# Optimization experiments

Measured on AMD Instinct MI355X. Metric: run time of the kernel, lower is better.

## Reference

```python
import jax, jax.numpy as jnp
import numpy as np

RUNS, WAYS, SHOT, QUERIES, D = 512, 5, 5, 15, 640
NS, QS = WAYS * SHOT, WAYS * QUERIES
LAM, ALPHA, UPDATE_RATE, EPOCHS = 10.0, 0.7, 0.6, 3
OT_EPS, OT_MAXITERS = 1e-3, 1000


def compute_entropy(P):
    # P: (runs, n, ways); normalized entropy per row
    P = P + 1e-12
    P = P / P.sum(axis=2, keepdims=True)
    H = -jnp.sum(P * jnp.log(P), axis=2)
    return H / jnp.log(jnp.asarray(P.shape[2], P.dtype))


def sq_cdist(a, b):
    # squared euclidean distance, (runs,n,d) x (runs,m,d) -> (runs,n,m)
    d2 = (a * a).sum(-1)[:, :, None] + (b * b).sum(-1)[:, None, :] \
         - 2.0 * jnp.einsum('bnd,bmd->bnm', a, b)
    return jnp.maximum(d2, 0.0)


def get_distance(f1, f2):
    return jnp.exp(-LAM * sq_cdist(f1, f2))


def build_graph(W):
    n = W.shape[1]
    W = W * (1.0 - jnp.eye(n, dtype=W.dtype)[None])  # zero diagonal
    Dm = W.sum(-1) ** -0.5                            # D^{-1/2}
    return Dm[:, None, :] * W * Dm[:, :, None]


def sinkhorn(M, n_l, labels, eps):
    # faithful port of compute_optimal_transport (class_balance=True)
    nr, n, ways = M.shape
    r = jnp.ones((nr, n), M.dtype)
    c = jnp.full((nr, ways), float(n // ways), M.dtype)  # ones*n//ways (floor)
    onehot = jax.nn.one_hot(labels[:, :n_l], ways, dtype=M.dtype) if n_l > 0 else None

    def cond(st):
        P, u, it = st
        return (jnp.max(jnp.abs(u - P.sum(2))) > eps) & (it <= OT_MAXITERS)

    def body(st):
        P, u, it = st
        u = P.sum(2)
        P = P * (r / u)[:, :, None]
        P = P * (c / P.sum(1))[:, None, :]
        if n_l > 0:
            P = P.at[:, :n_l, :].set(onehot)  # fill_(0) + scatter_(2, labels, 1)
        return P, u, it + 1

    P, _, _ = jax.lax.while_loop(cond, body, (M, jnp.zeros((nr, n), M.dtype), jnp.int32(1)))
    return P


def get_prob(features, proto, ys):
    d2 = sq_cdist(features, proto)
    Pq = jnp.exp(-LAM * d2[:, NS:])
    Pq = sinkhorn(Pq, 0, ys, 1e-3)
    Ps = jax.nn.one_hot(ys, WAYS, dtype=d2.dtype)  # scatter on support rows
    return jnp.concatenate([Ps, Pq], axis=1)


def _forward(xs, xq, ys, yq):
    features = jnp.concatenate([xs, xq], axis=1)           # (runs, ns+qs, d)
    labels = jnp.concatenate([ys, yq], axis=1)
    runs = features.shape[0]
    proto = features[:, :NS].reshape(runs, WAYS, SHOT, -1).mean(axis=2)
    Z = None
    for _ in range(EPOCHS):  # (pre-loop Z / Inverse_W in torch code are dead code)
        features = features[:, :NS + QS]
        Z = get_prob(features, proto, ys)
        ent = compute_entropy(Z)
        Z = Z * (1.0 - ent[..., None])
        # update_prototype
        new_proto = jnp.einsum('bnk,bnd->bkd', Z, features) / Z.sum(axis=1)[..., None]
        proto = (1.0 - UPDATE_RATE) * proto + UPDATE_RATE * new_proto
        dist_proto = get_distance(proto, proto)
        score = compute_entropy(dist_proto)
        omega = ent.mean(axis=1, keepdims=True)
        mask = (score < omega).astype(Z.dtype)             # (runs, ways)
        add_proto = proto * mask[..., None]
        dist_proto = dist_proto * mask[..., None]
        features = jnp.concatenate([features, add_proto], axis=1)  # (runs, ns+qs+ways, d)
        Z = jnp.concatenate([Z, dist_proto], axis=1)
        dist = get_distance(features, features)
        W = build_graph(dist)
        n = features.shape[1]
        Inv = jnp.linalg.inv(jnp.eye(n, dtype=W.dtype)[None] - ALPHA * W)
        Z = Inv @ Z                                         # (I - aW)^{-1} diffusion
        Z = sinkhorn(Z, NS, ys, OT_EPS)
    olabels = jnp.argmax(Z[:, :NS + QS], axis=2)
    matches = (labels == olabels).astype(jnp.float32)
    return matches[:, NS:].mean(axis=1)                     # acc_test: (runs,)


def setup_inputs() -> dict:
    key = jax.random.key(0)
    k1, k2, k3 = jax.random.split(key, 3)
    scale = 0.04  # keeps exp(-lam*dist^2) in fp32 normal range
    xs = scale * jax.random.normal(k1, (RUNS, NS, D), dtype=jnp.float32)
    xq = scale * jax.random.normal(k2, (RUNS, QS, D), dtype=jnp.float32)
    # support labels must be class-block ordered (proto reshape assumes it)
    ys = jnp.tile(jnp.repeat(jnp.arange(WAYS, dtype=jnp.int32), SHOT)[None, :], (RUNS, 1))
    yq = jax.random.randint(k3, (RUNS, QS), 0, WAYS, dtype=jnp.int32)
    return {'xs': xs, 'xq': xq, 'ys': ys, 'yq': yq}


def reference(xs, xq, ys, yq):
    return _forward(xs, xq, ys, yq)
```

## Files before the change

kernel.cpp:

```cpp
#include <hip/hip_runtime.h>
#include <math.h>

#define RUNS  512
#define WAYS  5
#define SHOT  5
#define NSUP  25
#define NQ    75
#define N0    100
#define NF    105
#define DIM   640
#define LAMB  10.0f
#define ALF   0.7f
#define UPD   0.6f
#define OT_EPSF 0.001f
#define OT_MAXIT 1000

#define NTILE 14
#define FCH_ROWS 112
#define FCH_STRIDE 36
#define HALF 56
#define CHUNK 64

struct __align__(16) Smem {
  float fch[FCH_ROWS * FCH_STRIDE];
  float pbuf[WAYS * DIM];
  float rowk[112];
  float colk[112];
  float Zm[NF * WAYS];
  float ent[NF];
  float fnorm[112];
  float dm[112];
  float rsumh[112];
  float dp[WAYS * WAYS];
  float pn[WAYS];
  float maskv[WAYS];
  float red[4];
  float pivotv;
  int foundsh;
  int ysl[NSUP];
};
static_assert(sizeof(Smem) <= 40 * 1024, "LDS: 2 blocks/CU (80KB of 160KB)");

__device__ __forceinline__ float wsum(float v) {
#pragma unroll
  for (int o = 32; o > 0; o >>= 1) v += __shfl_xor(v, o, 64);
  return v;
}
__device__ __forceinline__ float wmaxr(float v) {
#pragma unroll
  for (int o = 32; o > 0; o >>= 1) v = fmaxf(v, __shfl_xor(v, o, 64));
  return v;
}
__device__ __forceinline__ float bsum(float v, float* red, int tid) {
  v = wsum(v);
  __syncthreads();
  if ((tid & 63) == 0) red[tid >> 6] = v;
  __syncthreads();
  return (red[0] + red[1]) + (red[2] + red[3]);
}

__device__ __forceinline__ void gbar(unsigned* ctl, unsigned& bi, int tid, int r) {
  __syncthreads();
  if (tid == 0) {
    unsigned tgt = 8u * bi + 7u;
    bool flipped = false;
    unsigned a = __hip_atomic_fetch_add(&ctl[64 + (r >> 3)], 1u,
                                        __ATOMIC_RELEASE, __HIP_MEMORY_SCOPE_AGENT);
    if (a == tgt) {
      unsigned b = __hip_atomic_fetch_add(&ctl[128 + (r >> 6)], 1u,
                                          __ATOMIC_RELEASE, __HIP_MEMORY_SCOPE_AGENT);
      if (b == tgt) {
        unsigned c = __hip_atomic_fetch_add(&ctl[136], 1u,
                                            __ATOMIC_RELEASE, __HIP_MEMORY_SCOPE_AGENT);
        if (c == tgt) {
          __hip_atomic_store(&ctl[0], bi + 1u, __ATOMIC_RELEASE, __HIP_MEMORY_SCOPE_AGENT);
          flipped = true;
        }
      }
    }
    if (!flipped) {
      while (__hip_atomic_load(&ctl[0], __ATOMIC_RELAXED, __HIP_MEMORY_SCOPE_AGENT) != bi + 1u)
        __builtin_amdgcn_s_sleep(32);
    }
    bi++;
  }
  __syncthreads();
}

__device__ __forceinline__ float entropy5(const float* z) {
  float p[5]; float t = 0.f;
#pragma unroll
  for (int w = 0; w < 5; w++) { p[w] = z[w] + 1e-12f; t += p[w]; }
  float H = 0.f;
#pragma unroll
  for (int w = 0; w < 5; w++) { float q = p[w] / t; H -= q * logf(q); }
  return H / logf(5.0f);
}

__device__ __forceinline__ float loadF(const float* xs, const float* xq, int r, int i, int d) {
  return (i < NSUP) ? xs[(r * NSUP + i) * DIM + d] : xq[(r * NQ + (i - NSUP)) * DIM + d];
}

__device__ void sinkhorn_wave(Smem& sm, unsigned long long* orslots, unsigned* ctl,
                              unsigned& bi, int rowOff, int n, float cval,
                              bool clampLab, int tid, int r, int& sidx) {
  const int lane = tid & 63;
  const int wv = tid >> 6;
  float p0[5], p1[5], u0 = 0.f, u1 = 0.f;
  float q0[5], q1[5], v0 = 0.f, v1 = 0.f;
  bool e0 = false, e1 = false;
  int row0 = 0, y0 = -1;
  if (wv == 0) {
    row0 = lane;
    int row1 = lane + 64;
    e0 = row0 < n; e1 = row1 < n;
    y0 = (clampLab && row0 < NSUP) ? sm.ysl[row0] : -1;
#pragma unroll
    for (int w = 0; w < 5; w++) {
      p0[w] = e0 ? sm.Zm[(rowOff + row0) * 5 + w] : 0.f;
      p1[w] = e1 ? sm.Zm[(rowOff + row1) * 5 + w] : 0.f;
    }
  }
  auto body = [&]() {
    float t0 = 0.f, t1 = 0.f;
#pragma unroll
    for (int w = 0; w < 5; w++) { t0 += p0[w]; t1 += p1[w]; }
    u0 = t0; u1 = t1;
    float i0 = e0 ? 1.0f / t0 : 0.f;
    float i1 = e1 ? 1.0f / t1 : 0.f;
#pragma unroll
    for (int w = 0; w < 5; w++) { p0[w] *= i0; p1[w] *= i1; }
#pragma unroll
    for (int w = 0; w < 5; w++) {
      float cs = wsum(p0[w] + p1[w]);
      float f = cval / cs;
      p0[w] *= f; p1[w] *= f;
    }
    if (y0 >= 0) {
#pragma unroll
      for (int w = 0; w < 5; w++) p0[w] = (y0 == w) ? 1.0f : 0.0f;
    }
  };

  int base = 0;
  while (true) {
    unsigned long long mask = 0ull;
    if (wv == 0) {
#pragma unroll
      for (int w = 0; w < 5; w++) { q0[w] = p0[w]; q1[w] = p1[w]; }
      v0 = u0; v1 = u1;
#pragma unroll 1
      for (int p = 0; p < CHUNK; p++) {
        float t0 = 0.f, t1 = 0.f;
#pragma unroll
        for (int w = 0; w < 5; w++) { t0 += p0[w]; t1 += p1[w]; }
        float res = fmaxf(e0 ? fabsf(u0 - t0) : 0.f, e1 ? fabsf(u1 - t1) : 0.f);
        res = wmaxr(res);
        if (res > OT_EPSF) mask |= (1ull << p);
        body();
      }
      if (lane == 0)
        __hip_atomic_fetch_or(&orslots[(size_t)sidx * 8 + (r >> 6)], mask,
                              __ATOMIC_RELAXED, __HIP_MEMORY_SCOPE_AGENT);
    }
    gbar(ctl, bi, tid, r);
    if (tid == 0) {
      unsigned long long m = 0ull;
#pragma unroll
      for (int g = 0; g < 8; g++)
        m |= __hip_atomic_load(&orslots[(size_t)sidx * 8 + g], __ATOMIC_RELAXED,
                               __HIP_MEMORY_SCOPE_AGENT);
      int found = -1;
      for (int p = 0; p < CHUNK; p++) {
        int k = base + p + 1;
        bool cond = (((m >> p) & 1ull) != 0ull) && (k <= OT_MAXIT);
        if (!cond) { found = p; break; }
      }
      sm.foundsh = found;
    }
    __syncthreads();
    int found = sm.foundsh;
    sidx++;
    if (found >= 0) {
      if (wv == 0) {
#pragma unroll
        for (int w = 0; w < 5; w++) { p0[w] = q0[w]; p1[w] = q1[w]; }
        u0 = v0; u1 = v1;
#pragma unroll 1
        for (int p = 0; p < found; p++) body();
#pragma unroll
        for (int w = 0; w < 5; w++) {
          if (e0) sm.Zm[(rowOff + row0) * 5 + w] = p0[w];
          if (e1) sm.Zm[(rowOff + lane + 64) * 5 + w] = p1[w];
        }
      }
      __syncthreads();
      return;
    }
    base += CHUNK;
  }
}

__global__ void init_kernel(unsigned* __restrict__ ctl, float* __restrict__ out) {
  int i = blockIdx.x * blockDim.x + threadIdx.x;
  if (i < 4096) __hip_atomic_store(&ctl[i], 0u, __ATOMIC_RELAXED, __HIP_MEMORY_SCOPE_AGENT);
  if (i < RUNS) out[i] = -1.0f;
}

__global__ __launch_bounds__(256, 2) void fsl_kernel(
    const float* __restrict__ xs, const float* __restrict__ xq,
    const int* __restrict__ ys, const int* __restrict__ yq,
    float* __restrict__ out, unsigned* __restrict__ ctl) {
  __shared__ Smem sm;
  unsigned long long* orslots = (unsigned long long*)(ctl + 512);
  const int tid = threadIdx.x;
  const int r = blockIdx.x;
  const int lane = tid & 63, wid = tid >> 6;
  unsigned bi = 0;
  int sidx = 0;

  for (int i = wid; i < N0; i += 4) {
    float p = 0.f;
    for (int d = lane; d < DIM; d += 64) { float v = loadF(xs, xq, r, i, d); p += v * v; }
    p = wsum(p);
    if (lane == 0) sm.fnorm[i] = p;
  }
  if (tid < NSUP) sm.ysl[tid] = ys[r * NSUP + tid];
  for (int idx = tid; idx < WAYS * DIM; idx += 256) {
    int w = idx / DIM, d = idx % DIM;
    float sacc = 0.f;
#pragma unroll
    for (int s5 = 0; s5 < SHOT; s5++) sacc += xs[(r * NSUP + w * SHOT + s5) * DIM + d];
    sm.pbuf[idx] = sacc / 5.0f;
  }
  __syncthreads();

  int ti = 0, tj = 0;
  if (tid < 210) {
    int t = tid >> 1;
    while (t >= NTILE - ti) { t -= NTILE - ti; ti++; }
    tj = ti + t;
  }
  const int hcol = tid & 1;
  const bool own = tid < 210;
  const int erow = own ? (tid % 105) : 0;
  const int hh = own ? (tid / 105) : 0;
  const int jbase = HALF * hh;

  float (*band)[112] = (float (*)[112])sm.fch;

  for (int ep = 0; ep < 3; ep++) {
    for (int w = wid; w < WAYS; w += 4) {
      float p = 0.f;
      for (int d = lane; d < DIM; d += 64) { float v = sm.pbuf[w * DIM + d]; p += v * v; }
      p = wsum(p);
      if (lane == 0) sm.pn[w] = p;
    }
    __syncthreads();
    for (int pq = wid; pq < NQ * WAYS; pq += 4) {
      int q = pq / 5, w = pq % 5;
      float dt = 0.f;
      for (int d = lane; d < DIM; d += 64)
        dt += xq[(r * NQ + q) * DIM + d] * sm.pbuf[w * DIM + d];
      dt = wsum(dt);
      if (lane == 0) {
        float d2 = fmaxf(sm.fnorm[NSUP + q] + sm.pn[w] - 2.0f * dt, 0.0f);
        sm.Zm[(NSUP + q) * 5 + w] = expf(-LAMB * d2);
      }
    }
    __syncthreads();
    sinkhorn_wave(sm, orslots, ctl, bi, NSUP, NQ, 15.0f, false, tid, r, sidx);
    if (tid < NSUP * 5) { int i = tid / 5, w = tid % 5; sm.Zm[i * 5 + w] = (sm.ysl[i] == w) ? 1.0f : 0.0f; }
    __syncthreads();
    if (tid < N0) {
      float e = entropy5(&sm.Zm[tid * 5]);
      sm.ent[tid] = e;
      float f1 = 1.0f - e;
#pragma unroll
      for (int w = 0; w < 5; w++) sm.Zm[tid * 5 + w] *= f1;
    }
    __syncthreads();
    float zs[5];
#pragma unroll
    for (int w = 0; w < 5; w++) zs[w] = bsum(tid < N0 ? sm.Zm[tid * 5 + w] : 0.f, sm.red, tid);
    for (int d = tid; d < DIM; d += 256) {
      float a[5] = {0.f, 0.f, 0.f, 0.f, 0.f};
      for (int i = 0; i < N0; i++) {
        float v = loadF(xs, xq, r, i, d);
#pragma unroll
        for (int w = 0; w < 5; w++) a[w] += sm.Zm[i * 5 + w] * v;
      }
#pragma unroll
      for (int w = 0; w < 5; w++) {
        float old = sm.pbuf[w * DIM + d];
        sm.pbuf[w * DIM + d] = (1.0f - UPD) * old + UPD * (a[w] / zs[w]);
      }
    }
    __syncthreads();
    for (int w = wid; w < WAYS; w += 4) {
      float p = 0.f;
      for (int d = lane; d < DIM; d += 64) { float v = sm.pbuf[w * DIM + d]; p += v * v; }
      p = wsum(p);
      if (lane == 0) sm.pn[w] = p;
    }
    __syncthreads();
    for (int pp5 = wid; pp5 < 25; pp5 += 4) {
      int a5 = pp5 / 5, b5 = pp5 % 5;
      float dt = 0.f;
      for (int d = lane; d < DIM; d += 64)
        dt += sm.pbuf[a5 * DIM + d] * sm.pbuf[b5 * DIM + d];
      dt = wsum(dt);
      if (lane == 0) {
        float d2 = fmaxf(sm.pn[a5] + sm.pn[b5] - 2.0f * dt, 0.0f);
        sm.dp[pp5] = expf(-LAMB * d2);
      }
    }
    __syncthreads();
    float omega = bsum(tid < N0 ? sm.ent[tid] : 0.f, sm.red, tid) / 100.0f;
    if (tid < WAYS) {
      float sc = entropy5(&sm.dp[tid * 5]);
      sm.maskv[tid] = (sc < omega) ? 1.0f : 0.0f;
    }
    __syncthreads();
    if (tid < WAYS) sm.fnorm[N0 + tid] = sm.maskv[tid] * sm.pn[tid];
    if (tid < 25) { int a5 = tid / 5, b5 = tid % 5; sm.Zm[(N0 + a5) * 5 + b5] = sm.dp[tid] * sm.maskv[a5]; }
    __syncthreads();
    float acc[32];
#pragma unroll
    for (int z = 0; z < 32; z++) acc[z] = 0.f;
    for (int c = 0; c < 20; c++) {
      for (int idx = tid; idx < FCH_ROWS * 32; idx += 256) {
        int i = idx >> 5, dc = idx & 31;
        float v = 0.f;
        int d = c * 32 + dc;
        if (i < N0) v = loadF(xs, xq, r, i, d);
        else if (i < NF) v = sm.maskv[i - N0] * sm.pbuf[(i - N0) * DIM + d];
        int gg = dc >> 2, rm = dc & 3;
        sm.fch[i * FCH_STRIDE + (((gg ^ ((i >> 3) & 7)) << 2) | rm)] = v;
      }
      __syncthreads();
      if (tid < 210) {
        int i0 = ti * 8, j0 = tj * 8 + 4 * hcol, si = ti & 7, sj = tj & 7;
#pragma unroll
        for (int g = 0; g < 8; g++) {
          float4 a4[8], b4[4];
#pragma unroll
          for (int rr = 0; rr < 8; rr++)
            a4[rr] = *(const float4*)&sm.fch[(i0 + rr) * FCH_STRIDE + ((g ^ si) << 2)];
#pragma unroll
          for (int cc = 0; cc < 4; cc++)
            b4[cc] = *(const float4*)&sm.fch[(j0 + cc) * FCH_STRIDE + ((g ^ sj) << 2)];
#pragma unroll
          for (int rr = 0; rr < 8; rr++)
#pragma unroll
            for (int cc = 0; cc < 4; cc++)
              acc[rr * 4 + cc] += a4[rr].x * b4[cc].x + a4[rr].y * b4[cc].y +
                                  a4[rr].z * b4[cc].z + a4[rr].w * b4[cc].w;
        }
      }
      __syncthreads();
    }
    float Areg[HALF];
    float rsum = 0.f;
    for (int b = 0; b < NTILE; b++) {
      if (tid < 210) {
        if (ti == b) {
#pragma unroll
          for (int rr = 0; rr < 8; rr++)
#pragma unroll
            for (int cc = 0; cc < 4; cc++)
              band[rr][8 * tj + 4 * hcol + cc] = acc[rr * 4 + cc];
        }
        if (tj == b && ti != b) {
#pragma unroll
          for (int rr = 0; rr < 8; rr++)
#pragma unroll
            for (int cc = 0; cc < 4; cc++)
              band[4 * hcol + cc][8 * ti + rr] = acc[rr * 4 + cc];
        }
      }
      __syncthreads();
      if (own && (erow >> 3) == b) {
        int lr = erow & 7;
#pragma unroll
        for (int jj = 0; jj < HALF; jj++) {
          int j = jbase + jj;
          float wv = 0.f;
          if (j < NF && j != erow) {
            float d2 = fmaxf(sm.fnorm[erow] + sm.fnorm[j] - 2.0f * band[lr][j], 0.0f);
            wv = expf(-LAMB * d2);
          }
          Areg[jj] = wv;
          rsum += wv;
        }
      }
      __syncthreads();
    }
    if (own && hh == 1) sm.rsumh[erow] = rsum;
    __syncthreads();
    if (own && hh == 0) sm.dm[erow] = 1.0f / sqrtf(rsum + sm.rsumh[erow]);
    __syncthreads();
    float cnext = 0.f;
    if (own) {
      float dme = sm.dm[erow];
#pragma unroll
      for (int jj = 0; jj < HALF; jj++) {
        int j = jbase + jj;
        float t = (j < NF) ? (sm.dm[j] * Areg[jj]) * dme : 0.f;
        Areg[jj] = ((j == erow) ? 1.0f : 0.0f) - ALF * t;
      }
      if (hh == 0) cnext = Areg[0];
    }
    if (tid < 112) sm.rowk[tid] = 0.f;
    __syncthreads();
    for (int k = 0; k < NF; k++) {
      int hk = (k < HALF) ? 0 : 1;
      if (own && hh == hk) {
        if (erow == k) { sm.pivotv = cnext; sm.colk[k] = 0.f; }
        else sm.colk[erow] = cnext;
      }
      __syncthreads();
      float pinv = 1.0f / sm.pivotv;
      if (own && erow == k) {
#pragma unroll
        for (int jj = 0; jj < HALF; jj++) {
          int j = jbase + jj;
          if (j > k && j < NF) { Areg[jj] *= pinv; sm.rowk[j] = Areg[jj]; }
        }
        if (hh == hk) sm.rowk[k] = 0.f;
        if (hh == 0) {
#pragma unroll
          for (int w = 0; w < 5; w++) sm.Zm[k * 5 + w] *= pinv;
        }
      }
      __syncthreads();
      if (own) {
        float m = sm.colk[erow];
#pragma unroll
        for (int jj = 0; jj < HALF; jj += 4) {
          float4 rk = *(const float4*)&sm.rowk[jbase + jj];
          Areg[jj + 0] -= m * rk.x;
          Areg[jj + 1] -= m * rk.y;
          Areg[jj + 2] -= m * rk.z;
          Areg[jj + 3] -= m * rk.w;
        }
#pragma unroll
        for (int jj = 0; jj < HALF; jj++)
          if (jbase + jj == k + 1) cnext = Areg[jj];
        if (hh == 0 && erow != k) {
#pragma unroll
          for (int w = 0; w < 5; w++) sm.Zm[erow * 5 + w] -= m * sm.Zm[k * 5 + w];
        }
      }
      __syncthreads();
    }
    sinkhorn_wave(sm, orslots, ctl, bi, 0, NF, 21.0f, true, tid, r, sidx);
  }

  float mt = 0.f;
  if (tid < NQ) {
    int row = NSUP + tid;
    float best = sm.Zm[row * 5]; int bl = 0;
#pragma unroll
    for (int w = 1; w < 5; w++) { float v = sm.Zm[row * 5 + w]; if (v > best) { best = v; bl = w; } }
    mt = (yq[r * NQ + tid] == bl) ? 1.0f : 0.0f;
  }
  float tot = bsum(mt, sm.red, tid);
  if (tid == 0) out[r] = tot / 75.0f;
}

extern "C" void kernel_launch(void* const* d_in, const int* in_sizes, int n_in,
                              void* d_out, int out_size, void* d_ws, size_t ws_size,
                              hipStream_t stream) {
  const float* xs = (const float*)d_in[0];
  const float* xq = (const float*)d_in[1];
  const int* ys = (const int*)d_in[2];
  const int* yq = (const int*)d_in[3];
  float* out = (float*)d_out;
  unsigned* ctl = (unsigned*)d_ws;
  init_kernel<<<dim3(16), dim3(256), 0, stream>>>(ctl, out);
  fsl_kernel<<<dim3(RUNS), dim3(256), 0, stream>>>(xs, xq, ys, yq, out, ctl);
}
```

Baseline: 7.105 ms.

## Fuse convergence check into grid barrier root and broadcast result via padded wake words

```diff
diff --git a/kernel.cpp b/kernel.cpp
--- a/kernel.cpp
+++ b/kernel.cpp
@@ -20,6 +20,12 @@
 #define FCH_STRIDE 36
 #define HALF 56
 #define CHUNK 64
+
+#define W_WAKE(g)  ((g) * 16)
+#define W_C1(g)    (1024 + (g) * 16)
+#define W_C2(s)    (2048 + (s) * 16)
+#define W_C0       2176
+#define W_SLOT(b,g) (2304 + ((b) * 16 + (g)) * 16)
 
 struct __align__(16) Smem {
   float fch[FCH_ROWS * FCH_STRIDE];
@@ -59,29 +65,55 @@
   return (red[0] + red[1]) + (red[2] + red[3]);
 }
 
-__device__ __forceinline__ void gbar(unsigned* ctl, unsigned& bi, int tid, int r) {
+__device__ __forceinline__ void gbar_found(Smem& sm, unsigned* ctl, unsigned& bi,
+                                           int tid, int r, int buf, int base) {
   __syncthreads();
   if (tid == 0) {
-    unsigned tgt = 8u * bi + 7u;
-    bool flipped = false;
-    unsigned a = __hip_atomic_fetch_add(&ctl[64 + (r >> 3)], 1u,
+    const unsigned tgt = 8u * bi + 7u;
+    const unsigned seq = bi + 1u;
+    int found = -1;
+    bool isroot = false;
+    unsigned a = __hip_atomic_fetch_add(&ctl[W_C1(r >> 3)], 1u,
                                         __ATOMIC_RELEASE, __HIP_MEMORY_SCOPE_AGENT);
     if (a == tgt) {
-      unsigned b = __hip_atomic_fetch_add(&ctl[128 + (r >> 6)], 1u,
+      unsigned b = __hip_atomic_fetch_add(&ctl[W_C2(r >> 6)], 1u,
                                           __ATOMIC_RELEASE, __HIP_MEMORY_SCOPE_AGENT);
       if (b == tgt) {
-        unsigned c = __hip_atomic_fetch_add(&ctl[136], 1u,
+        unsigned c = __hip_atomic_fetch_add(&ctl[W_C0], 1u,
                                             __ATOMIC_RELEASE, __HIP_MEMORY_SCOPE_AGENT);
-        if (c == tgt) {
-          __hip_atomic_store(&ctl[0], bi + 1u, __ATOMIC_RELEASE, __HIP_MEMORY_SCOPE_AGENT);
-          flipped = true;
-        }
-      }
-    }
-    if (!flipped) {
-      while (__hip_atomic_load(&ctl[0], __ATOMIC_RELAXED, __HIP_MEMORY_SCOPE_AGENT) != bi + 1u)
-        __builtin_amdgcn_s_sleep(32);
-    }
+        if (c == tgt) isroot = true;
+      }
+    }
+    if (isroot) {
+      unsigned long long m = 0ull;
+#pragma unroll
+      for (int g = 0; g < 16; g++)
+        m |= __hip_atomic_load((unsigned long long*)(ctl + W_SLOT(buf, g)),
+                               __ATOMIC_RELAXED, __HIP_MEMORY_SCOPE_AGENT);
+      for (int p = 0; p < CHUNK; p++) {
+        int k = base + p + 1;
+        bool cond = (((m >> p) & 1ull) != 0ull) && (k <= OT_MAXIT);
+        if (!cond) { found = p; break; }
+      }
+#pragma unroll
+      for (int g = 0; g < 16; g++)
+        __hip_atomic_store((unsigned long long*)(ctl + W_SLOT(buf, g)), 0ull,
+                           __ATOMIC_RELAXED, __HIP_MEMORY_SCOPE_AGENT);
+      unsigned pk = seq | ((unsigned)(found + 1) << 16);
+      __hip_atomic_store(&ctl[W_WAKE(0)], pk, __ATOMIC_RELEASE, __HIP_MEMORY_SCOPE_AGENT);
+#pragma unroll 4
+      for (int g = 1; g < 64; g++)
+        __hip_atomic_store(&ctl[W_WAKE(g)], pk, __ATOMIC_RELAXED, __HIP_MEMORY_SCOPE_AGENT);
+    } else {
+      unsigned w;
+      for (;;) {
+        w = __hip_atomic_load(&ctl[W_WAKE(r >> 3)], __ATOMIC_RELAXED, __HIP_MEMORY_SCOPE_AGENT);
+        if ((w & 0xffffu) >= seq) break;
+        __builtin_amdgcn_s_sleep(8);
+      }
+      found = (int)((w >> 16) & 0xffu) - 1;
+    }
+    sm.foundsh = found;
     bi++;
   }
   __syncthreads();
@@ -101,7 +133,7 @@
   return (i < NSUP) ? xs[(r * NSUP + i) * DIM + d] : xq[(r * NQ + (i - NSUP)) * DIM + d];
 }
 
-__device__ void sinkhorn_wave(Smem& sm, unsigned long long* orslots, unsigned* ctl,
+__device__ void sinkhorn_wave(Smem& sm, unsigned* ctl,
                               unsigned& bi, int rowOff, int n, float cval,
                               bool clampLab, int tid, int r, int& sidx) {
   const int lane = tid & 63;
@@ -160,25 +192,10 @@
         body();
       }
       if (lane == 0)
-        __hip_atomic_fetch_or(&orslots[(size_t)sidx * 8 + (r >> 6)], mask,
+        __hip_atomic_fetch_or((unsigned long long*)(ctl + W_SLOT(sidx & 1, r >> 5)), mask,
                               __ATOMIC_RELAXED, __HIP_MEMORY_SCOPE_AGENT);
     }
-    gbar(ctl, bi, tid, r);
-    if (tid == 0) {
-      unsigned long long m = 0ull;
-#pragma unroll
-      for (int g = 0; g < 8; g++)
-        m |= __hip_atomic_load(&orslots[(size_t)sidx * 8 + g], __ATOMIC_RELAXED,
-                               __HIP_MEMORY_SCOPE_AGENT);
-      int found = -1;
-      for (int p = 0; p < CHUNK; p++) {
-        int k = base + p + 1;
-        bool cond = (((m >> p) & 1ull) != 0ull) && (k <= OT_MAXIT);
-        if (!cond) { found = p; break; }
-      }
-      sm.foundsh = found;
-    }
-    __syncthreads();
+    gbar_found(sm, ctl, bi, tid, r, sidx & 1, base);
     int found = sm.foundsh;
     sidx++;
     if (found >= 0) {
@@ -212,7 +229,6 @@
     const int* __restrict__ ys, const int* __restrict__ yq,
     float* __restrict__ out, unsigned* __restrict__ ctl) {
   __shared__ Smem sm;
-  unsigned long long* orslots = (unsigned long long*)(ctl + 512);
   const int tid = threadIdx.x;
   const int r = blockIdx.x;
   const int lane = tid & 63, wid = tid >> 6;
@@ -269,7 +285,7 @@
       }
     }
     __syncthreads();
-    sinkhorn_wave(sm, orslots, ctl, bi, NSUP, NQ, 15.0f, false, tid, r, sidx);
+    sinkhorn_wave(sm, ctl, bi, NSUP, NQ, 15.0f, false, tid, r, sidx);
     if (tid < NSUP * 5) { int i = tid / 5, w = tid % 5; sm.Zm[i * 5 + w] = (sm.ysl[i] == w) ? 1.0f : 0.0f; }
     __syncthreads();
     if (tid < N0) {
@@ -454,7 +470,7 @@
       }
       __syncthreads();
     }
-    sinkhorn_wave(sm, orslots, ctl, bi, 0, NF, 21.0f, true, tid, r, sidx);
+    sinkhorn_wave(sm, ctl, bi, 0, NF, 21.0f, true, tid, r, sidx);
   }
 
   float mt = 0.f;
```

Result: slower. 7.256 ms (+2.1%).
